# Kernel optimization log

Measured on AMD Instinct MI355X. Metric: run time of the kernel, lower is better.

Reference implementation:

```python
import jax, jax.numpy as jnp
import numpy as np

B, H, S, D = 2, 16, 2048, 64  # batch, heads, seq_len, depth (F_hidden)
EPS_ADJ = 1e-09
NEG_INF = -1000000000.0


def iswiglu(x):
    # x * silu(x) == x^2 * sigmoid(x), always >= 0
    return x * jax.nn.silu(x)


def setup_inputs() -> dict:
    key = jax.random.key(0)
    ks = jax.random.split(key, 8)
    Hin = jax.random.normal(ks[0], (B, H, S, D), jnp.float32)
    Hk = jax.random.normal(ks[1], (B, H, S, D), jnp.float32)
    Hv = jax.random.normal(ks[2], (B, H, S, D), jnp.float32)
    A = jax.random.normal(ks[3], (B, H, D, D), jnp.float32)
    # causal (look-ahead) mask: 1 where attention is disallowed
    mask = jnp.triu(jnp.ones((S, S), jnp.float32), k=1)[None, None, :, :]
    xavier = np.sqrt(2.0 / (D + D)).astype(np.float32)  # xavier_normal gain=1 for [D,D] fans
    W = jax.random.normal(ks[4], (H, D, D), jnp.float32) * xavier
    pw = jax.random.normal(ks[5], (H, D, D), jnp.float32) * xavier
    a = jax.random.normal(ks[6], (H, D, D), jnp.float32) * xavier
    b = jnp.zeros((H, D, D), jnp.float32)
    ba = jnp.zeros((H, D, D), jnp.float32)
    return {"Hin": Hin, "Hk": Hk, "Hv": Hv, "A": A, "mask": mask,
            "W": W, "b": b, "pw": pw, "a": a, "ba": ba}


def reference(Hin, Hk, Hv, A, mask, W, b, pw, a, ba):
    # metric-tensor transform: AW = iSwiGLU(W @ A + b) + eps   [B,H,D,D]
    x = jnp.einsum('hij,bhjk->bhik', W, A) + b[None]
    AW = iswiglu(x) + EPS_ADJ
    # energy-curvature tensor: avAp = a @ AW**pw + ba           [B,H,D,D]
    Ap = jnp.power(AW, pw[None])
    avAp = jnp.einsum('hij,bhjk->bhik', a, Ap) + ba[None]
    # bilinear attention scores: (Hin @ avAp) @ Hk^T / sqrt(D)  [B,H,S,S]
    q = jnp.matmul(Hin, avAp)
    Ep = jnp.matmul(q, jnp.swapaxes(Hk, -1, -2)) / jnp.sqrt(jnp.float32(D))
    E = jax.nn.softmax(Ep + mask * NEG_INF, axis=-1)
    Hout = jnp.matmul(E, Hv)                                   # [B,H,S,D]
    return Hout
```

## Files before the change

### kernel.cpp

```cpp
#include <hip/hip_runtime.h>


typedef short v8s __attribute__((ext_vector_type(8)));
typedef float v4f __attribute__((ext_vector_type(4)));

__device__ __forceinline__ float bf2f(unsigned short u) {
    union { unsigned int i; float f; } v; v.i = ((unsigned int)u) << 16; return v.f;
}
__device__ __forceinline__ unsigned short f2bf(float f) {
    unsigned int u = __float_as_uint(f);
    u += 0x7fffu + ((u >> 16) & 1u);
    return (unsigned short)(u >> 16);
}
__device__ __forceinline__ v4f mfma16(v8s a, v8s b, v4f c) {
    return __builtin_amdgcn_mfma_f32_16x16x32_bf16(a, b, c, 0, 0, 0);
}
__device__ __forceinline__ void gload_lds16(const void* g, void* l) {
    __builtin_amdgcn_global_load_lds(
        (const __attribute__((address_space(1))) void*)g,
        (__attribute__((address_space(3))) void*)l, 16, 0, 0);
}
__device__ __forceinline__ void block_sync() {
    asm volatile("" ::: "memory");
    __builtin_amdgcn_s_barrier();
    asm volatile("" ::: "memory");
}

__global__ __launch_bounds__(256)
void pre1_kernel(const float* __restrict__ A,  const float* __restrict__ W,
                 const float* __restrict__ b,  const float* __restrict__ pw,
                 float* __restrict__ Pbuf)
{
    __shared__ float sA[4096], sW[512];
    const int bx = blockIdx.x, bh = blockIdx.y, h = bh & 15, t = threadIdx.x;
    const int lcol = t & 63, lrow = t >> 6, r0 = bx * 8;
    for (int i = t; i < 4096; i += 256) sA[i] = A[bh*4096 + i];
    for (int i = t; i < 512;  i += 256) sW[i] = W[h*4096 + r0*64 + i];
    __syncthreads();
    double acc[2];
    #pragma unroll
    for (int e = 0; e < 2; ++e)
        acc[e] = (double)b[h*4096 + (r0 + lrow + 4*e)*64 + lcol];
    #pragma unroll 4
    for (int jj = 0; jj < 16; ++jj) {
        double a0 = (double)sA[(4*jj+0)*64 + lcol];
        double a1 = (double)sA[(4*jj+1)*64 + lcol];
        double a2 = (double)sA[(4*jj+2)*64 + lcol];
        double a3 = (double)sA[(4*jj+3)*64 + lcol];
        #pragma unroll
        for (int e = 0; e < 2; ++e) {
            const float* wr = &sW[(lrow + 4*e)*64 + 4*jj];
            acc[e] += (double)wr[0]*a0 + (double)wr[1]*a1
                    + (double)wr[2]*a2 + (double)wr[3]*a3;
        }
    }
    #pragma unroll
    for (int e = 0; e < 2; ++e) {
        int idx = (r0 + lrow + 4*e)*64 + lcol;
        double v = acc[e];
        double sig = 1.0 / (1.0 + exp(-v));
        Pbuf[bh*4096 + idx] = (float)pow(v*v*sig + 1e-9, (double)pw[h*4096 + idx]);
    }
}

__global__ __launch_bounds__(256)
void pre2_kernel(const float* __restrict__ a,  const float* __restrict__ ba,
                 const float* __restrict__ Pbuf, float* __restrict__ avap)
{
    __shared__ float sP[4096], sa[512];
    const int bx = blockIdx.x, bh = blockIdx.y, h = bh & 15, t = threadIdx.x;
    const int lcol = t & 63, lrow = t >> 6, r0 = bx * 8;
    for (int i = t; i < 4096; i += 256) sP[i] = Pbuf[bh*4096 + i];
    for (int i = t; i < 512;  i += 256) sa[i] = a[h*4096 + r0*64 + i];
    __syncthreads();
    double acc[2];
    #pragma unroll
    for (int e = 0; e < 2; ++e)
        acc[e] = (double)ba[h*4096 + (r0 + lrow + 4*e)*64 + lcol];
    #pragma unroll 4
    for (int jj = 0; jj < 16; ++jj) {
        double a0 = (double)sP[(4*jj+0)*64 + lcol];
        double a1 = (double)sP[(4*jj+1)*64 + lcol];
        double a2 = (double)sP[(4*jj+2)*64 + lcol];
        double a3 = (double)sP[(4*jj+3)*64 + lcol];
        #pragma unroll
        for (int e = 0; e < 2; ++e) {
            const float* wr = &sa[(lrow + 4*e)*64 + 4*jj];
            acc[e] += (double)wr[0]*a0 + (double)wr[1]*a1
                    + (double)wr[2]*a2 + (double)wr[3]*a3;
        }
    }
    #pragma unroll
    for (int e = 0; e < 2; ++e)
        avap[bh*4096 + (r0 + lrow + 4*e)*64 + lcol] = (float)acc[e];
}

__global__ __launch_bounds__(256)
void pre_legacy(const float* __restrict__ A,  const float* __restrict__ W,
                const float* __restrict__ b,  const float* __restrict__ pw,
                const float* __restrict__ a,  const float* __restrict__ ba,
                float* __restrict__ avap)
{
    __shared__ float sW[4096], sA[4096], sP[4096];
    const int bh = blockIdx.x, h = bh & 15, t = threadIdx.x;
    const int lcol = t & 63, lrow = t >> 6;
    for (int i = t; i < 4096; i += 256) { sW[i] = W[h*4096+i]; sA[i] = A[bh*4096+i]; }
    __syncthreads();
    {
        double acc[16];
        #pragma unroll
        for (int e = 0; e < 16; ++e)
            acc[e] = (double)b[h*4096 + (lrow + 4*e)*64 + lcol];
        #pragma unroll 4
        for (int jj = 0; jj < 16; ++jj) {
            double a0 = (double)sA[(4*jj+0)*64 + lcol];
            double a1 = (double)sA[(4*jj+1)*64 + lcol];
            double a2 = (double)sA[(4*jj+2)*64 + lcol];
            double a3 = (double)sA[(4*jj+3)*64 + lcol];
            #pragma unroll
            for (int e = 0; e < 16; ++e) {
                const float* wr = &sW[(lrow + 4*e)*64 + 4*jj];
                acc[e] += (double)wr[0]*a0 + (double)wr[1]*a1
                        + (double)wr[2]*a2 + (double)wr[3]*a3;
            }
        }
        #pragma unroll
        for (int e = 0; e < 16; ++e) {
            int idx = (lrow + 4*e)*64 + lcol;
            double v = acc[e];
            double sig = 1.0 / (1.0 + exp(-v));
            sP[idx] = (float)pow(v*v*sig + 1e-9, (double)pw[h*4096 + idx]);
        }
    }
    __syncthreads();
    for (int i = t; i < 4096; i += 256) sW[i] = a[h*4096+i];
    __syncthreads();
    {
        double acc[16];
        #pragma unroll
        for (int e = 0; e < 16; ++e)
            acc[e] = (double)ba[h*4096 + (lrow + 4*e)*64 + lcol];
        #pragma unroll 4
        for (int jj = 0; jj < 16; ++jj) {
            double a0 = (double)sP[(4*jj+0)*64 + lcol];
            double a1 = (double)sP[(4*jj+1)*64 + lcol];
            double a2 = (double)sP[(4*jj+2)*64 + lcol];
            double a3 = (double)sP[(4*jj+3)*64 + lcol];
            #pragma unroll
            for (int e = 0; e < 16; ++e) {
                const float* wr = &sW[(lrow + 4*e)*64 + 4*jj];
                acc[e] += (double)wr[0]*a0 + (double)wr[1]*a1
                        + (double)wr[2]*a2 + (double)wr[3]*a3;
            }
        }
        #pragma unroll
        for (int e = 0; e < 16; ++e)
            avap[bh*4096 + (lrow + 4*e)*64 + lcol] = (float)acc[e];
    }
}

__global__ __launch_bounds__(256)
void q_mfma(const float* __restrict__ Hin, const float* __restrict__ avap,
            float* __restrict__ qout)
{
    __shared__ __align__(16) unsigned short s[16384];
    const int qt = blockIdx.x, bh = blockIdx.y, t = threadIdx.x;
    const int w = t >> 6, lane = t & 63, l15 = lane & 15, quad = lane >> 4;
    const int base = bh*131072 + qt*4096;
    #pragma unroll
    for (int i = 0; i < 16; ++i) {
        int p = t + 256*i;
        int r = p >> 6, k = p & 63;
        float v = Hin[base + p];
        unsigned short h = f2bf(v);
        int addr = r*64 + (((((k>>3) ^ (r&7))) << 3) | (k & 7));
        s[addr] = h;
        s[4096 + addr] = f2bf(v - bf2f(h));
    }
    #pragma unroll
    for (int i = 0; i < 16; ++i) {
        int p = t + 256*i;
        int k = p >> 6, n = p & 63;
        float v = avap[bh*4096 + p];
        unsigned short h = f2bf(v);
        int addr = n*64 + (((((k>>3) ^ (n&7))) << 3) | (k & 7));
        s[8192 + addr] = h;
        s[12288 + addr] = f2bf(v - bf2f(h));
    }
    __syncthreads();
    const int sl = (quad ^ (l15 & 7)) << 3;
    const int aoff = (16*w + l15)*64 + sl;
    v8s ahi0 = *(const v8s*)&s[aoff];
    v8s ahi1 = *(const v8s*)&s[aoff ^ 32];
    v8s alo0 = *(const v8s*)&s[4096 + aoff];
    v8s alo1 = *(const v8s*)&s[4096 + (aoff ^ 32)];
    #pragma unroll
    for (int nt = 0; nt < 4; ++nt) {
        const int boff = 8192 + (16*nt + l15)*64 + sl;
        v8s bhi0 = *(const v8s*)&s[boff];
        v8s bhi1 = *(const v8s*)&s[boff ^ 32];
        v8s blo0 = *(const v8s*)&s[4096 + boff];
        v8s blo1 = *(const v8s*)&s[4096 + (boff ^ 32)];
        v4f acc = (v4f){0,0,0,0};
        acc = mfma16(alo0, bhi0, acc);
        acc = mfma16(alo1, bhi1, acc);
        acc = mfma16(ahi0, blo0, acc);
        acc = mfma16(ahi1, blo1, acc);
        acc = mfma16(ahi0, bhi0, acc);
        acc = mfma16(ahi1, bhi1, acc);
        #pragma unroll
        for (int reg = 0; reg < 4; ++reg)
            qout[base + (16*w + quad*4 + reg)*64 + 16*nt + l15] = acc[reg] * 0.125f;
    }
}

__global__ __launch_bounds__(256)
void q_kernel(const float* __restrict__ Hin, const float* __restrict__ avap,
              float* __restrict__ qout)
{
    __shared__ float sH[4096], sAv[4096];
    const int qt = blockIdx.x, bh = blockIdx.y, t = threadIdx.x;
    const int lcol = t & 63, lrow = t >> 6;
    const int base = bh*131072 + qt*4096;
    for (int i = t; i < 4096; i += 256) { sH[i] = Hin[base+i]; sAv[i] = avap[bh*4096+i]; }
    __syncthreads();
    float acc[16];
    #pragma unroll
    for (int e = 0; e < 16; ++e) acc[e] = 0.0f;
    #pragma unroll 4
    for (int jj = 0; jj < 16; ++jj) {
        float a0 = sAv[(4*jj+0)*64 + lcol];
        float a1 = sAv[(4*jj+1)*64 + lcol];
        float a2 = sAv[(4*jj+2)*64 + lcol];
        float a3 = sAv[(4*jj+3)*64 + lcol];
        #pragma unroll
        for (int e = 0; e < 16; ++e) {
            const float* hr = &sH[(lrow + 4*e)*64 + 4*jj];
            acc[e] += hr[0]*a0 + hr[1]*a1 + hr[2]*a2 + hr[3]*a3;
        }
    }
    #pragma unroll
    for (int e = 0; e < 16; ++e)
        qout[base + (lrow + 4*e)*64 + lcol] = acc[e] * 0.125f;
}

__global__ __launch_bounds__(256)
void kvprep_kernel(const float* __restrict__ Hk, const float* __restrict__ Hv,
                   unsigned short* __restrict__ kv)
{
    __shared__ __align__(16) unsigned short sVT[4096];
    const int kt = blockIdx.x, bh = blockIdx.y, t = threadIdx.x;
    const float* hk = Hk + bh*131072 + kt*4096;
    const float* hv = Hv + bh*131072 + kt*4096;
    unsigned short* dst = kv + (size_t)(bh*32 + kt) * 12288;

    #pragma unroll
    for (int it = 0; it < 2; ++it) {
        int item = t + 256*it;
        int kr = item >> 3, oc = item & 7;
        const float* src = hk + kr*64 + oc*8;
        float4 g0 = *(const float4*)(src);
        float4 g1 = *(const float4*)(src + 4);
        float fv[8] = {g0.x,g0.y,g0.z,g0.w,g1.x,g1.y,g1.z,g1.w};
        v8s hi, lo;
        #pragma unroll
        for (int j = 0; j < 8; ++j) {
            unsigned short h = f2bf(fv[j]);
            hi[j] = (short)h;
            lo[j] = (short)f2bf(fv[j] - bf2f(h));
        }
        int addr = kr*64 + ((oc ^ (kr & 7)) << 3);
        *(v8s*)(dst + addr) = hi;
        *(v8s*)(dst + 4096 + addr) = lo;
    }
    #pragma unroll
    for (int i = 0; i < 16; ++i) {
        int p = t + 256*i;
        int kr = p >> 6, d = p & 63;
        sVT[d*64 + (((((kr>>3) ^ (d&7))) << 3) | (kr & 7))] = f2bf(hv[p]);
    }
    __syncthreads();
    #pragma unroll
    for (int i = 0; i < 2; ++i)
        ((uint4*)(dst + 8192))[t + 256*i] = ((const uint4*)sVT)[t + 256*i];
}

#define TILE_HW 12288
#define PBASE   24576

__global__ __launch_bounds__(512, 4)
void attn_kernel(const unsigned short* __restrict__ kv, float* __restrict__ io)
{
    __shared__ __align__(16) unsigned short sm16[32768];
    const int t    = threadIdx.x;
    const int w    = t >> 6;
    const int wq   = w & 3;
    const int lane = t & 63;
    const int l15  = lane & 15;
    const int quad = lane >> 4;
    const int x    = blockIdx.x;
    const int bh   = blockIdx.y;
    const int bhb  = bh * 131072;
    const int qt_a = x, qt_b = 31 - x;
    const int qsel = (w < 4) ? qt_a : qt_b;
    const int q0   = qsel * 64;
    const char* kvb = (const char*)(kv + (size_t)bh * 32 * TILE_HW);

    const float* qrow = io + bhb + (q0 + 16*wq + l15)*64 + quad*8;
    float4 f0 = *(const float4*)(qrow);
    float4 f1 = *(const float4*)(qrow + 4);
    float4 f2 = *(const float4*)(qrow + 32);
    float4 f3 = *(const float4*)(qrow + 36);

    #pragma unroll
    for (int j = 0; j < 3; ++j) {
        int c = 3*w + j;
        gload_lds16(kvb + c*1024 + (size_t)lane*16, (char*)sm16 + c*1024);
    }

    v8s qhi[2], qlo[2];
    {
        float fv0[8] = {f0.x,f0.y,f0.z,f0.w,f1.x,f1.y,f1.z,f1.w};
        float fv1[8] = {f2.x,f2.y,f2.z,f2.w,f3.x,f3.y,f3.z,f3.w};
        #pragma unroll
        for (int j = 0; j < 8; ++j) {
            unsigned short h0 = f2bf(fv0[j]);
            qhi[0][j] = (short)h0; qlo[0][j] = (short)f2bf(fv0[j] - bf2f(h0));
            unsigned short h1 = f2bf(fv1[j]);
            qhi[1][j] = (short)h1; qlo[1][j] = (short)f2bf(fv1[j] - bf2f(h1));
        }
    }

    v4f O[4];
    float m_[4], l_[4];
    #pragma unroll
    for (int i = 0; i < 4; ++i) { O[i] = (v4f){0,0,0,0}; m_[i] = -1e30f; l_[i] = 0.0f; }

    const int sl = (quad ^ (l15 & 7)) << 3;

    for (int kt = 0; kt <= qt_b; ++kt) {
        const int base = (kt & 1) * TILE_HW;
        if (kt < qt_b) {
            const char* gs = kvb + (size_t)(kt+1) * (TILE_HW*2);
            char* lb = (char*)sm16 + ((kt+1) & 1) * (TILE_HW*2);
            #pragma unroll
            for (int j = 0; j < 3; ++j) {
                int c = 3*w + j;
                gload_lds16(gs + c*1024 + (size_t)lane*16, lb + c*1024);
            }
            asm volatile("s_waitcnt vmcnt(3)" ::: "memory");
        } else {
            asm volatile("s_waitcnt vmcnt(0)" ::: "memory");
        }
        block_sync();

        if (kt <= qsel) {
            v4f s[4];
            #pragma unroll
            for (int ct = 0; ct < 4; ++ct) {
                const int kb = base + (16*ct + l15)*64 + sl;
                v8s kh0 = *(const v8s*)&sm16[kb];
                v8s kh1 = *(const v8s*)&sm16[kb ^ 32];
                v8s kl0 = *(const v8s*)&sm16[kb + 4096];
                v8s kl1 = *(const v8s*)&sm16[(kb ^ 32) + 4096];
                v4f a = (v4f){0,0,0,0};
                a = mfma16(qlo[0], kh0, a);
                a = mfma16(qlo[1], kh1, a);
                a = mfma16(qhi[0], kl0, a);
                a = mfma16(qhi[1], kl1, a);
                a = mfma16(qhi[0], kh0, a);
                a = mfma16(qhi[1], kh1, a);
                s[ct] = a;
            }

            if (kt == qsel) {
                #pragma unroll
                for (int ct = 0; ct < 4; ++ct)
                    #pragma unroll
                    for (int r = 0; r < 4; ++r)
                        if (16*ct + l15 > 16*wq + quad*4 + r) s[ct][r] = -1e30f;
            }

            float pv[4][4];
            #pragma unroll
            for (int reg = 0; reg < 4; ++reg) {
                float rm = fmaxf(fmaxf(s[0][reg], s[1][reg]), fmaxf(s[2][reg], s[3][reg]));
                rm = fmaxf(rm, __shfl_xor(rm, 1));
                rm = fmaxf(rm, __shfl_xor(rm, 2));
                rm = fmaxf(rm, __shfl_xor(rm, 4));
                rm = fmaxf(rm, __shfl_xor(rm, 8));
                float mn = fmaxf(m_[reg], rm);
                float al = __expf(m_[reg] - mn);
                m_[reg] = mn;
                float rs = 0.0f;
                #pragma unroll
                for (int ct = 0; ct < 4; ++ct) {
                    float e = __expf(s[ct][reg] - mn);
                    pv[ct][reg] = e; rs += e;
                }
                rs += __shfl_xor(rs, 1);
                rs += __shfl_xor(rs, 2);
                rs += __shfl_xor(rs, 4);
                rs += __shfl_xor(rs, 8);
                l_[reg] = l_[reg]*al + rs;
                #pragma unroll
                for (int d = 0; d < 4; ++d) O[d][reg] *= al;
            }

            #pragma unroll
            for (int reg = 0; reg < 4; ++reg) {
                const int row = quad*4 + reg;
                #pragma unroll
                for (int ct = 0; ct < 4; ++ct)
                    sm16[PBASE + w*1024 + row*64 +
                         ((((2*ct + (l15 >> 3)) ^ (row & 7)) << 3) | (l15 & 7))]
                        = f2bf(pv[ct][reg]);
            }
            asm volatile("s_waitcnt lgkmcnt(0)" ::: "memory");

            const int pb = PBASE + w*1024 + l15*64 + sl;
            v8s pA0 = *(const v8s*)&sm16[pb];
            v8s pA1 = *(const v8s*)&sm16[pb ^ 32];
            #pragma unroll
            for (int d = 0; d < 4; ++d) {
                const int vb = base + 8192 + (16*d + l15)*64 + sl;
                v8s v0 = *(const v8s*)&sm16[vb];
                v8s v1 = *(const v8s*)&sm16[vb ^ 32];
                O[d] = mfma16(pA0, v0, O[d]);
                O[d] = mfma16(pA1, v1, O[d]);
            }
        }
        asm volatile("s_waitcnt lgkmcnt(0)" ::: "memory");
        block_sync();
    }

    #pragma unroll
    for (int reg = 0; reg < 4; ++reg) {
        float inv = 1.0f / l_[reg];
        int row = q0 + 16*wq + quad*4 + reg;
        #pragma unroll
        for (int d = 0; d < 4; ++d)
            io[bhb + row*64 + 16*d + l15] = O[d][reg] * inv;
    }
}

#define KHI 0
#define KLO 4608
#define VTB 9216
#define PB  13824

__global__ __launch_bounds__(256, 4)
void attn_legacy(const float* __restrict__ Hk, const float* __restrict__ Hv,
                 float* __restrict__ io)
{
    __shared__ __align__(16) unsigned short sm16[18432];
    const int t    = threadIdx.x;
    const int w    = t >> 6;
    const int lane = t & 63;
    const int l15  = lane & 15;
    const int quad = lane >> 4;
    const int x    = blockIdx.x;
    const int bh   = blockIdx.y;
    const int bhb  = bh * 131072;

    for (int pass = 0; pass < 2; ++pass) {
        const int qt = pass ? (31 - x) : x;
        const int q0 = qt * 64;

        v8s qhi[2], qlo[2];
        {
            const float* qr = io + bhb + (q0 + 16*w + l15)*64 + quad*8;
            #pragma unroll
            for (int ks = 0; ks < 2; ++ks)
                #pragma unroll
                for (int j = 0; j < 8; ++j) {
                    float qv = qr[32*ks + j];
                    unsigned short h = f2bf(qv);
                    unsigned short l = f2bf(qv - bf2f(h));
                    qhi[ks][j] = (short)h; qlo[ks][j] = (short)l;
                }
        }

        v4f O[4];
        float m_[4], l_[4];
        #pragma unroll
        for (int i = 0; i < 4; ++i) { O[i] = (v4f){0,0,0,0}; m_[i] = -1e30f; l_[i] = 0.0f; }

        for (int kt = 0; kt <= qt; ++kt) {
            __syncthreads();
            const int tb = bhb + kt*4096;
            #pragma unroll 4
            for (int i = 0; i < 16; ++i) {
                int p = t + 256*i;
                int kr = p >> 6, d = p & 63;
                float kvv = Hk[tb + p];
                unsigned short h = f2bf(kvv);
                sm16[KHI + kr*72 + d] = h;
                sm16[KLO + kr*72 + d] = f2bf(kvv - bf2f(h));
                sm16[VTB + d*72 + kr] = f2bf(Hv[tb + p]);
            }
            __syncthreads();

            v4f s[4];
            #pragma unroll
            for (int ct = 0; ct < 4; ++ct) {
                const unsigned short* kb = &sm16[(16*ct + l15)*72 + quad*8];
                v8s kh0 = *(const v8s*)(kb + KHI);
                v8s kh1 = *(const v8s*)(kb + KHI + 32);
                v8s kl0 = *(const v8s*)(kb + KLO);
                v8s kl1 = *(const v8s*)(kb + KLO + 32);
                v4f a = (v4f){0,0,0,0};
                a = mfma16(qlo[0], kh0, a);
                a = mfma16(qlo[1], kh1, a);
                a = mfma16(qhi[0], kl0, a);
                a = mfma16(qhi[1], kl1, a);
                a = mfma16(qhi[0], kh0, a);
                a = mfma16(qhi[1], kh1, a);
                s[ct] = a;
            }

            if (kt == qt) {
                #pragma unroll
                for (int ct = 0; ct < 4; ++ct)
                    #pragma unroll
                    for (int r = 0; r < 4; ++r)
                        if (16*ct + l15 > 16*w + quad*4 + r) s[ct][r] = -1e30f;
            }

            float pv[4][4];
            #pragma unroll
            for (int reg = 0; reg < 4; ++reg) {
                float rm = fmaxf(fmaxf(s[0][reg], s[1][reg]), fmaxf(s[2][reg], s[3][reg]));
                rm = fmaxf(rm, __shfl_xor(rm, 1));
                rm = fmaxf(rm, __shfl_xor(rm, 2));
                rm = fmaxf(rm, __shfl_xor(rm, 4));
                rm = fmaxf(rm, __shfl_xor(rm, 8));
                float mn = fmaxf(m_[reg], rm);
                float al = __expf(m_[reg] - mn);
                m_[reg] = mn;
                float rs = 0.0f;
                #pragma unroll
                for (int ct = 0; ct < 4; ++ct) {
                    float e = __expf(s[ct][reg] - mn);
                    pv[ct][reg] = e; rs += e;
                }
                rs += __shfl_xor(rs, 1);
                rs += __shfl_xor(rs, 2);
                rs += __shfl_xor(rs, 4);
                rs += __shfl_xor(rs, 8);
                l_[reg] = l_[reg]*al + rs;
                #pragma unroll
                for (int d = 0; d < 4; ++d) O[d][reg] *= al;
            }

            #pragma unroll
            for (int reg = 0; reg < 4; ++reg)
                #pragma unroll
                for (int ct = 0; ct < 4; ++ct)
                    sm16[PB + w*1152 + (quad*4+reg)*72 + 16*ct + l15] = f2bf(pv[ct][reg]);
            asm volatile("s_waitcnt lgkmcnt(0)" ::: "memory");

            const unsigned short* pb = &sm16[PB + w*1152 + l15*72 + quad*8];
            v8s pA0 = *(const v8s*)(pb);
            v8s pA1 = *(const v8s*)(pb + 32);
            #pragma unroll
            for (int d = 0; d < 4; ++d) {
                const unsigned short* vb = &sm16[VTB + (16*d + l15)*72 + quad*8];
                v8s v0 = *(const v8s*)(vb);
                v8s v1 = *(const v8s*)(vb + 32);
                O[d] = mfma16(pA0, v0, O[d]);
                O[d] = mfma16(pA1, v1, O[d]);
            }
        }

        #pragma unroll
        for (int reg = 0; reg < 4; ++reg) {
            float inv = 1.0f / l_[reg];
            int row = q0 + 16*w + quad*4 + reg;
            #pragma unroll
            for (int d = 0; d < 4; ++d)
                io[bhb + row*64 + 16*d + l15] = O[d][reg] * inv;
        }
        __syncthreads();
    }
}

extern "C" void kernel_launch(void* const* d_in, const int* in_sizes, int n_in,
                              void* d_out, int out_size, void* d_ws, size_t ws_size,
                              hipStream_t stream)
{
    const float* Hin = (const float*)d_in[0];
    const float* Hk  = (const float*)d_in[1];
    const float* Hv  = (const float*)d_in[2];
    const float* A   = (const float*)d_in[3];
    const float* W   = (const float*)d_in[5];
    const float* b   = (const float*)d_in[6];
    const float* pw  = (const float*)d_in[7];
    const float* a   = (const float*)d_in[8];
    const float* ba  = (const float*)d_in[9];
    float* out  = (float*)d_out;
    float* avap = (float*)d_ws;

    const size_t KVOFF = 1u << 20;
    const size_t NEED  = KVOFF + (size_t)1024 * 24576;

    if (ws_size >= NEED) {
        float* Pbuf = (float*)((char*)d_ws + (512u << 10));
        unsigned short* kvb = (unsigned short*)((char*)d_ws + KVOFF);
        pre1_kernel<<<dim3(8, 32), dim3(256), 0, stream>>>(A, W, b, pw, Pbuf);
        pre2_kernel<<<dim3(8, 32), dim3(256), 0, stream>>>(a, ba, Pbuf, avap);
        kvprep_kernel<<<dim3(32, 32), dim3(256), 0, stream>>>(Hk, Hv, kvb);
        q_mfma<<<dim3(32, 32), dim3(256), 0, stream>>>(Hin, avap, out);
        attn_kernel<<<dim3(16, 32), dim3(512), 0, stream>>>(kvb, out);
    } else {
        pre_legacy<<<dim3(32), dim3(256), 0, stream>>>(A, W, b, pw, a, ba, avap);
        q_kernel<<<dim3(32, 32), dim3(256), 0, stream>>>(Hin, avap, out);
        attn_legacy<<<dim3(16, 32), dim3(256), 0, stream>>>(Hk, Hv, out);
    }
}
```

Before: 212.5 us.

## Fuse Q projection into attention kernel and use exp2 with prescaled logits

Removes the separate q_mfma launch: the attention kernel now loads Hin rows and avAp into LDS, computes q via split-bf16 MFMA, folds log2(e)/sqrt(D) into the scale, and stores q back to LDS as hi/lo bf16 before the main loop. Softmax exponentials switch from __expf to raw v_exp_f32 (exp2), which is consistent with the prescale. The grid is flattened to 1D with a remapped block index to change scheduling and L2 locality. kvprep's V transpose is reworked to use float4 loads into a rotated float LDS tile and vectorized bf16 stores. This saves a launch and a global round trip for q, at the cost of extra prologue work and LDS traffic in every attention block.

```diff
diff --git a/kernel.cpp b/kernel.cpp
--- a/kernel.cpp
+++ b/kernel.cpp
@@ -24,6 +24,11 @@
     asm volatile("" ::: "memory");
     __builtin_amdgcn_s_barrier();
     asm volatile("" ::: "memory");
+}
+__device__ __forceinline__ float fexp2(float x) {
+    float r;
+    asm volatile("v_exp_f32 %0, %1" : "=v"(r) : "v"(x));
+    return r;
 }
 
 __global__ __launch_bounds__(256)
@@ -160,61 +165,6 @@
 }
 
 __global__ __launch_bounds__(256)
-void q_mfma(const float* __restrict__ Hin, const float* __restrict__ avap,
-            float* __restrict__ qout)
-{
-    __shared__ __align__(16) unsigned short s[16384];
-    const int qt = blockIdx.x, bh = blockIdx.y, t = threadIdx.x;
-    const int w = t >> 6, lane = t & 63, l15 = lane & 15, quad = lane >> 4;
-    const int base = bh*131072 + qt*4096;
-    #pragma unroll
-    for (int i = 0; i < 16; ++i) {
-        int p = t + 256*i;
-        int r = p >> 6, k = p & 63;
-        float v = Hin[base + p];
-        unsigned short h = f2bf(v);
-        int addr = r*64 + (((((k>>3) ^ (r&7))) << 3) | (k & 7));
-        s[addr] = h;
-        s[4096 + addr] = f2bf(v - bf2f(h));
-    }
-    #pragma unroll
-    for (int i = 0; i < 16; ++i) {
-        int p = t + 256*i;
-        int k = p >> 6, n = p & 63;
-        float v = avap[bh*4096 + p];
-        unsigned short h = f2bf(v);
-        int addr = n*64 + (((((k>>3) ^ (n&7))) << 3) | (k & 7));
-        s[8192 + addr] = h;
-        s[12288 + addr] = f2bf(v - bf2f(h));
-    }
-    __syncthreads();
-    const int sl = (quad ^ (l15 & 7)) << 3;
-    const int aoff = (16*w + l15)*64 + sl;
-    v8s ahi0 = *(const v8s*)&s[aoff];
-    v8s ahi1 = *(const v8s*)&s[aoff ^ 32];
-    v8s alo0 = *(const v8s*)&s[4096 + aoff];
-    v8s alo1 = *(const v8s*)&s[4096 + (aoff ^ 32)];
-    #pragma unroll
-    for (int nt = 0; nt < 4; ++nt) {
-        const int boff = 8192 + (16*nt + l15)*64 + sl;
-        v8s bhi0 = *(const v8s*)&s[boff];
-        v8s bhi1 = *(const v8s*)&s[boff ^ 32];
-        v8s blo0 = *(const v8s*)&s[4096 + boff];
-        v8s blo1 = *(const v8s*)&s[4096 + (boff ^ 32)];
-        v4f acc = (v4f){0,0,0,0};
-        acc = mfma16(alo0, bhi0, acc);
-        acc = mfma16(alo1, bhi1, acc);
-        acc = mfma16(ahi0, blo0, acc);
-        acc = mfma16(ahi1, blo1, acc);
-        acc = mfma16(ahi0, bhi0, acc);
-        acc = mfma16(ahi1, bhi1, acc);
-        #pragma unroll
-        for (int reg = 0; reg < 4; ++reg)
-            qout[base + (16*w + quad*4 + reg)*64 + 16*nt + l15] = acc[reg] * 0.125f;
-    }
-}
-
-__global__ __launch_bounds__(256)
 void q_kernel(const float* __restrict__ Hin, const float* __restrict__ avap,
               float* __restrict__ qout)
 {
@@ -248,7 +198,7 @@
 void kvprep_kernel(const float* __restrict__ Hk, const float* __restrict__ Hv,
                    unsigned short* __restrict__ kv)
 {
-    __shared__ __align__(16) unsigned short sVT[4096];
+    __shared__ float sV[4096];
     const int kt = blockIdx.x, bh = blockIdx.y, t = threadIdx.x;
     const float* hk = Hk + bh*131072 + kt*4096;
     const float* hv = Hv + bh*131072 + kt*4096;
@@ -274,22 +224,40 @@
         *(v8s*)(dst + 4096 + addr) = lo;
     }
     #pragma unroll
-    for (int i = 0; i < 16; ++i) {
-        int p = t + 256*i;
-        int kr = p >> 6, d = p & 63;
-        sVT[d*64 + (((((kr>>3) ^ (d&7))) << 3) | (kr & 7))] = f2bf(hv[p]);
+    for (int i = 0; i < 4; ++i) {
+        int idx = t + 256*i;
+        int kr = idx >> 4, d0 = (idx & 15) * 4;
+        float4 g = *(const float4*)(hv + kr*64 + d0);
+        float gv[4] = {g.x, g.y, g.z, g.w};
+        #pragma unroll
+        for (int j = 0; j < 4; ++j)
+            sV[kr*64 + ((d0 + j + kr) & 63)] = gv[j];
     }
     __syncthreads();
     #pragma unroll
-    for (int i = 0; i < 2; ++i)
-        ((uint4*)(dst + 8192))[t + 256*i] = ((const uint4*)sVT)[t + 256*i];
+    for (int it = 0; it < 2; ++it) {
+        int item = t + 256*it;
+        int d = item >> 3, oc = item & 7;
+        v8s o;
+        #pragma unroll
+        for (int j = 0; j < 8; ++j) {
+            int kr = oc*8 + j;
+            o[j] = (short)f2bf(sV[kr*64 + ((d + kr) & 63)]);
+        }
+        *(v8s*)(dst + 8192 + d*64 + ((oc ^ (d & 7)) << 3)) = o;
+    }
 }
 
 #define TILE_HW 12288
 #define PBASE   24576
+#define QLO     8192
+#define AVT     16384
 
 __global__ __launch_bounds__(512, 4)
-void attn_kernel(const unsigned short* __restrict__ kv, float* __restrict__ io)
+void attn_kernel(const unsigned short* __restrict__ kv,
+                 const float* __restrict__ Hin,
+                 const float* __restrict__ avap,
+                 float* __restrict__ io)
 {
     __shared__ __align__(16) unsigned short sm16[32768];
     const int t    = threadIdx.x;
@@ -298,19 +266,88 @@
     const int lane = t & 63;
     const int l15  = lane & 15;
     const int quad = lane >> 4;
-    const int x    = blockIdx.x;
-    const int bh   = blockIdx.y;
+    const int g    = (blockIdx.x & 7) * 64 + (blockIdx.x >> 3);
+    const int bh   = g >> 4;
+    const int x    = g & 15;
     const int bhb  = bh * 131072;
     const int qt_a = x, qt_b = 31 - x;
     const int qsel = (w < 4) ? qt_a : qt_b;
     const int q0   = qsel * 64;
     const char* kvb = (const char*)(kv + (size_t)bh * 32 * TILE_HW);
-
-    const float* qrow = io + bhb + (q0 + 16*wq + l15)*64 + quad*8;
-    float4 f0 = *(const float4*)(qrow);
-    float4 f1 = *(const float4*)(qrow + 4);
-    float4 f2 = *(const float4*)(qrow + 32);
-    float4 f3 = *(const float4*)(qrow + 36);
+    const int sl   = (quad ^ (l15 & 7)) << 3;
+    const int wrow0 = (w < 4) ? wq*16 : 64 + wq*16;
+
+    #pragma unroll
+    for (int i = 0; i < 16; ++i) {
+        int p = t + 512*i;
+        int r = p >> 6, c = p & 63;
+        int grow = (r < 64) ? (qt_a*64 + r) : (qt_b*64 + (r - 64));
+        float v = Hin[bhb + grow*64 + c];
+        unsigned short h = f2bf(v);
+        int ad = r*64 + ((((c >> 3) ^ (r & 7)) << 3) | (c & 7));
+        sm16[ad] = h;
+        sm16[QLO + ad] = f2bf(v - bf2f(h));
+    }
+    #pragma unroll
+    for (int i = 0; i < 8; ++i) {
+        int p = t + 512*i;
+        int k = p >> 6, n = p & 63;
+        float v = avap[bh*4096 + p];
+        unsigned short h = f2bf(v);
+        int ad = n*64 + ((((k >> 3) ^ (n & 7)) << 3) | (k & 7));
+        sm16[AVT + ad] = h;
+        sm16[AVT + 4096 + ad] = f2bf(v - bf2f(h));
+    }
+    asm volatile("s_waitcnt lgkmcnt(0)" ::: "memory");
+    block_sync();
+
+    v4f qacc[4];
+    {
+        const int aoff = (wrow0 + l15)*64 + sl;
+        v8s ahi0 = *(const v8s*)&sm16[aoff];
+        v8s ahi1 = *(const v8s*)&sm16[aoff ^ 32];
+        v8s alo0 = *(const v8s*)&sm16[QLO + aoff];
+        v8s alo1 = *(const v8s*)&sm16[QLO + (aoff ^ 32)];
+        #pragma unroll
+        for (int nt = 0; nt < 4; ++nt) {
+            const int bo = (16*nt + l15)*64 + sl;
+            v8s bhi0 = *(const v8s*)&sm16[AVT + bo];
+            v8s bhi1 = *(const v8s*)&sm16[AVT + (bo ^ 32)];
+            v8s blo0 = *(const v8s*)&sm16[AVT + 4096 + bo];
+            v8s blo1 = *(const v8s*)&sm16[AVT + 4096 + (bo ^ 32)];
+            v4f acc = (v4f){0,0,0,0};
+            acc = mfma16(alo0, bhi0, acc);
+            acc = mfma16(alo1, bhi1, acc);
+            acc = mfma16(ahi0, blo0, acc);
+            acc = mfma16(ahi1, blo1, acc);
+            acc = mfma16(ahi0, bhi0, acc);
+            acc = mfma16(ahi1, bhi1, acc);
+            qacc[nt] = acc;
+        }
+    }
+    #pragma unroll
+    for (int nt = 0; nt < 4; ++nt)
+        #pragma unroll
+        for (int reg = 0; reg < 4; ++reg) {
+            float v = qacc[nt][reg] * 0.1803368801111244f;
+            int row = wrow0 + quad*4 + reg;
+            int col = 16*nt + l15;
+            int ad = row*64 + ((((col >> 3) ^ (row & 7)) << 3) | (col & 7));
+            unsigned short h = f2bf(v);
+            sm16[ad] = h;
+            sm16[QLO + ad] = f2bf(v - bf2f(h));
+        }
+    asm volatile("s_waitcnt lgkmcnt(0)" ::: "memory");
+    v8s qhi[2], qlo[2];
+    {
+        const int aoff = (wrow0 + l15)*64 + sl;
+        qhi[0] = *(const v8s*)&sm16[aoff];
+        qhi[1] = *(const v8s*)&sm16[aoff ^ 32];
+        qlo[0] = *(const v8s*)&sm16[QLO + aoff];
+        qlo[1] = *(const v8s*)&sm16[QLO + (aoff ^ 32)];
+    }
+    asm volatile("s_waitcnt lgkmcnt(0)" ::: "memory");
+    block_sync();
 
     #pragma unroll
     for (int j = 0; j < 3; ++j) {
@@ -318,25 +355,10 @@
         gload_lds16(kvb + c*1024 + (size_t)lane*16, (char*)sm16 + c*1024);
     }
 
-    v8s qhi[2], qlo[2];
-    {
-        float fv0[8] = {f0.x,f0.y,f0.z,f0.w,f1.x,f1.y,f1.z,f1.w};
-        float fv1[8] = {f2.x,f2.y,f2.z,f2.w,f3.x,f3.y,f3.z,f3.w};
-        #pragma unroll
-        for (int j = 0; j < 8; ++j) {
-            unsigned short h0 = f2bf(fv0[j]);
-            qhi[0][j] = (short)h0; qlo[0][j] = (short)f2bf(fv0[j] - bf2f(h0));
-            unsigned short h1 = f2bf(fv1[j]);
-            qhi[1][j] = (short)h1; qlo[1][j] = (short)f2bf(fv1[j] - bf2f(h1));
-        }
-    }
-
     v4f O[4];
     float m_[4], l_[4];
     #pragma unroll
     for (int i = 0; i < 4; ++i) { O[i] = (v4f){0,0,0,0}; m_[i] = -1e30f; l_[i] = 0.0f; }
-
-    const int sl = (quad ^ (l15 & 7)) << 3;
 
     for (int kt = 0; kt <= qt_b; ++kt) {
         const int base = (kt & 1) * TILE_HW;
@@ -390,12 +412,12 @@
                 rm = fmaxf(rm, __shfl_xor(rm, 4));
                 rm = fmaxf(rm, __shfl_xor(rm, 8));
                 float mn = fmaxf(m_[reg], rm);
-                float al = __expf(m_[reg] - mn);
+                float al = fexp2(m_[reg] - mn);
                 m_[reg] = mn;
                 float rs = 0.0f;
                 #pragma unroll
                 for (int ct = 0; ct < 4; ++ct) {
-                    float e = __expf(s[ct][reg] - mn);
+                    float e = fexp2(s[ct][reg] - mn);
                     pv[ct][reg] = e; rs += e;
                 }
                 rs += __shfl_xor(rs, 1);
@@ -610,8 +632,7 @@
         pre1_kernel<<<dim3(8, 32), dim3(256), 0, stream>>>(A, W, b, pw, Pbuf);
         pre2_kernel<<<dim3(8, 32), dim3(256), 0, stream>>>(a, ba, Pbuf, avap);
         kvprep_kernel<<<dim3(32, 32), dim3(256), 0, stream>>>(Hk, Hv, kvb);
-        q_mfma<<<dim3(32, 32), dim3(256), 0, stream>>>(Hin, avap, out);
-        attn_kernel<<<dim3(16, 32), dim3(512), 0, stream>>>(kvb, out);
+        attn_kernel<<<dim3(512), dim3(512), 0, stream>>>(kvb, Hin, avap, out);
     } else {
         pre_legacy<<<dim3(32), dim3(256), 0, stream>>>(A, W, b, pw, a, ba, avap);
         q_kernel<<<dim3(32, 32), dim3(256), 0, stream>>>(Hin, avap, out);
```

Result: faster. 206.3 us (-2.9%).
